# Kernel tuning notes

Hardware: AMD Instinct MI355X
Metric: run time of the kernel (lower is better)

## Reference

```python
import jax, jax.numpy as jnp
import numpy as np

EMBED = 768
HEADS = 12
HEAD_DIM = EMBED // HEADS


def setup_inputs() -> dict:
    key = jax.random.key(0)
    ks = jax.random.split(key, 9)
    B, S, E = 2, 2048, EMBED
    scale = 1.0 / np.sqrt(E)
    return {
        "query": jax.random.normal(ks[0], (B, S, E), jnp.float32),
        "key": jax.random.normal(ks[1], (B, S, E), jnp.float32),
        "value": jax.random.normal(ks[2], (B, S, E), jnp.float32),
        # nn.Linear weights are [out, in]; applied as x @ W.T + b
        "Wq": jax.random.normal(ks[3], (E, E), jnp.float32) * scale,
        "bq": jax.random.normal(ks[4], (E,), jnp.float32) * 0.01,
        "Wk": jax.random.normal(ks[5], (E, E), jnp.float32) * scale,
        "bk": jax.random.normal(ks[6], (E,), jnp.float32) * 0.01,
        "Wv": jax.random.normal(ks[7], (E, E), jnp.float32) * scale,
        "bv": jax.random.normal(ks[8], (E,), jnp.float32) * 0.01,
    }


def reference(query, key, value, Wq, bq, Wk, bk, Wv, bv):
    B, S, E = query.shape
    H, D = HEADS, HEAD_DIM
    # QKV projections (nn.Linear: x @ W.T + b), split into heads
    Q = (query @ Wq.T + bq).reshape(B, S, H, D)
    K = (key @ Wk.T + bk).reshape(B, S, H, D)
    V = (value @ Wv.T + bv).reshape(B, S, H, D)
    # hand-rolled attention: scores -> softmax -> weighted sum
    scores = jnp.einsum("bqhd,bkhd->bhqk", Q, K) / jnp.sqrt(jnp.float32(D))
    attn = jax.nn.softmax(scores, axis=-1)
    out = jnp.einsum("bhqk,bkhd->bqhd", attn, V).reshape(B, S, E)
    return out
```

## Files before the change

kernel.cpp:

```cpp
#include <hip/hip_runtime.h>

#define LOG2E 1.4426950408889634f
#define NEGC (-5.0f * LOG2E)

typedef _Float16 half2v __attribute__((ext_vector_type(2)));
typedef _Float16 half4v __attribute__((ext_vector_type(4)));
typedef _Float16 half8v __attribute__((ext_vector_type(8)));
typedef float float4v __attribute__((ext_vector_type(4)));
typedef float float16v __attribute__((ext_vector_type(16)));
typedef unsigned int uint4v __attribute__((ext_vector_type(4)));

#define NX (2 * 2048 * 768)
#define NW (768 * 768)
#define PO_SPLIT (24 * 2048 * 64)

__device__ __forceinline__ void gload_lds16(const _Float16* g, _Float16* l) {
    __builtin_amdgcn_global_load_lds((const __attribute__((address_space(1))) void*)g,
                                     (__attribute__((address_space(3))) void*)l, 16, 0, 0);
}

__global__ __launch_bounds__(256) void cvt6(
    const float* __restrict__ x0, const float* __restrict__ x1, const float* __restrict__ x2,
    const float* __restrict__ w0, const float* __restrict__ w1, const float* __restrict__ w2,
    _Float16* __restrict__ y0, _Float16* __restrict__ y1, _Float16* __restrict__ y2,
    _Float16* __restrict__ y3, _Float16* __restrict__ y4, _Float16* __restrict__ y5)
{
    const int z = blockIdx.y;
    const float* s; _Float16* d; int n;
    switch (z) {
        case 0: s = x0; d = y0; n = NX; break;
        case 1: s = x1; d = y1; n = NX; break;
        case 2: s = x2; d = y2; n = NX; break;
        case 3: s = w0; d = y3; n = NW; break;
        case 4: s = w1; d = y4; n = NW; break;
        default: s = w2; d = y5; n = NW; break;
    }
    const int i = (blockIdx.x * 256 + threadIdx.x) * 8;
    if (i >= n) return;
    float4v a0 = ((const float4v*)(s + i))[0];
    float4v a1 = ((const float4v*)(s + i))[1];
    half8v h = __builtin_shufflevector(__builtin_convertvector(a0, half4v),
                                       __builtin_convertvector(a1, half4v),
                                       0, 1, 2, 3, 4, 5, 6, 7);
    *(half8v*)(d + i) = h;
}

template<int TM, int TN, int AM, int AN, int MODE>
__global__ __launch_bounds__(256) void gemm16(
    const _Float16* __restrict__ Aq, const _Float16* __restrict__ Ak,
    const _Float16* __restrict__ Bq, const _Float16* __restrict__ Bk,
    const float* __restrict__ biasq, const float* __restrict__ biask,
    _Float16* __restrict__ Oq, _Float16* __restrict__ Ok)
{
    const int z = (MODE == 0) ? blockIdx.z : 0;
    const _Float16* A = z ? Ak : Aq;
    const _Float16* B = z ? Bk : Bq;
    const float* bias = z ? biask : biasq;

    __shared__ _Float16 At[TM * 64];
    __shared__ _Float16 Bt[TN * 64];

    const int t    = threadIdx.x;
    const int wave = t >> 6;
    const int lane = t & 63;
    const int quad = lane >> 4;
    const int l16  = lane & 15;
    const int wm   = (wave & 1) * (AM * 16);
    const int wn   = (wave >> 1) * (AN * 16);
    const int m0   = blockIdx.x * TM;
    const int n0   = blockIdx.y * TN;

    float4v acc[AM][AN];
#pragma unroll
    for (int i = 0; i < AM; i++)
#pragma unroll
        for (int j = 0; j < AN; j++) acc[i][j] = (float4v){0.f, 0.f, 0.f, 0.f};

    const _Float16* Asrc = A + (size_t)m0 * 768;
    const _Float16* Bsrc = B + (size_t)n0 * 768;

    for (int k0 = 0; k0 < 768; k0 += 64) {
#pragma unroll
        for (int j = 0; j < TM / 32; j++) {
            const int s = j * 256 + t;
            const int row = s >> 3;
            const int c = (s & 7) ^ (row & 7);
            gload_lds16(Asrc + (size_t)row * 768 + k0 + c * 8, At + s * 8);
        }
#pragma unroll
        for (int j = 0; j < TN / 32; j++) {
            const int s = j * 256 + t;
            const int row = s >> 3;
            const int c = (s & 7) ^ (row & 7);
            gload_lds16(Bsrc + (size_t)row * 768 + k0 + c * 8, Bt + s * 8);
        }
        __syncthreads();

        half8v af[AM][2], bf[AN][2];
#pragma unroll
        for (int i = 0; i < AM; i++) {
            const int ra = wm + i * 16 + l16;
            const int ca = quad ^ (ra & 7);
            af[i][0] = *(const half8v*)(At + ra * 64 + ca * 8);
            af[i][1] = *(const half8v*)(At + ra * 64 + (ca ^ 4) * 8);
        }
#pragma unroll
        for (int j = 0; j < AN; j++) {
            const int rb = wn + j * 16 + l16;
            const int cb = quad ^ (rb & 7);
            bf[j][0] = *(const half8v*)(Bt + rb * 64 + cb * 8);
            bf[j][1] = *(const half8v*)(Bt + rb * 64 + (cb ^ 4) * 8);
        }
#pragma unroll
        for (int i = 0; i < AM; i++)
#pragma unroll
            for (int j = 0; j < AN; j++) {
                acc[i][j] = __builtin_amdgcn_mfma_f32_16x16x32_f16(af[i][0], bf[j][0], acc[i][j], 0, 0, 0);
                acc[i][j] = __builtin_amdgcn_mfma_f32_16x16x32_f16(af[i][1], bf[j][1], acc[i][j], 0, 0, 0);
            }
        __syncthreads();
    }

    if (MODE == 0) {
        _Float16* O = z ? Ok : Oq;
        const float scale = z ? 1.0f : 0.125f * LOG2E;
#pragma unroll
        for (int j = 0; j < AN; j++) {
            const int col = n0 + wn + j * 16 + l16;
            const float bc = bias[col];
#pragma unroll
            for (int i = 0; i < AM; i++) {
                const int rowb = m0 + wm + i * 16 + quad * 4;
#pragma unroll
                for (int r = 0; r < 4; r++)
                    O[(size_t)(rowb + r) * 768 + col] = (_Float16)((acc[i][j][r] + bc) * scale);
            }
        }
    } else {
#pragma unroll
        for (int i = 0; i < AM; i++) {
#pragma unroll
            for (int r = 0; r < 4; r++) {
                const int m = m0 + wm + i * 16 + quad * 4 + r;
                const float bc = bias[m];
#pragma unroll
                for (int j = 0; j < AN; j++) {
                    const int n = n0 + wn + j * 16 + l16;
                    Oq[((size_t)(n >> 11) * 768 + m) * 2048 + (n & 2047)] = (_Float16)(acc[i][j][r] + bc);
                }
            }
        }
    }
}

__global__ __launch_bounds__(256) void attn3(
    const _Float16* __restrict__ Qh,
    const _Float16* __restrict__ Kh,
    const _Float16* __restrict__ Vt,
    _Float16* __restrict__ Po,
    float* __restrict__ lo)
{
    __shared__ _Float16 smem[4][64 * 64];

    const int t    = threadIdx.x;
    const int wave = t >> 6;
    const int lane = t & 63;
    const int hi   = lane >> 5;
    const int l32  = lane & 31;
    const int q0   = blockIdx.x * 128;
    const int bh   = blockIdx.y;
    const int sp   = blockIdx.z;
    const int b    = bh / 12;
    const int h    = bh % 12;
    const int qw   = q0 + wave * 32;

    const _Float16* qp = Qh + (size_t)(b * 2048 + qw + l32) * 768 + h * 64 + hi * 8;
    half8v qf[4];
#pragma unroll
    for (int d = 0; d < 4; d++) qf[d] = *(const half8v*)(qp + d * 16);

    float16v ot[2];
#pragma unroll
    for (int dc = 0; dc < 2; dc++)
#pragma unroll
        for (int r = 0; r < 16; r++) ot[dc][r] = 0.f;
    float lpart = 0.f;

    const _Float16* Kbase = Kh + (size_t)(b * 2048 + sp * 1024) * 768 + h * 64;
    const _Float16* Vbase = Vt + (size_t)(bh * 64) * 2048 + sp * 1024;

    auto stage = [&](int pp, int kt0) {
#pragma unroll
        for (int j = 0; j < 2; j++) {
            const int s = j * 256 + t;
            const int row = s >> 3;
            const int cg = (s & 7) ^ (row & 7);
            gload_lds16(Kbase + (size_t)(kt0 + row) * 768 + cg * 8, &smem[pp][s * 8]);
            gload_lds16(Vbase + (size_t)row * 2048 + kt0 + cg * 8, &smem[2 + pp][s * 8]);
        }
    };

    stage(0, 0);
    int p = 0;

    for (int it = 0; it < 16; it++) {
        __syncthreads();
        if (it < 15) stage(p ^ 1, (it + 1) * 64);

        float16v st[2];
#pragma unroll
        for (int kc = 0; kc < 2; kc++)
#pragma unroll
            for (int r = 0; r < 16; r++) st[kc][r] = 0.f;
#pragma unroll
        for (int ds = 0; ds < 4; ds++) {
#pragma unroll
            for (int kc = 0; kc < 2; kc++) {
                const int row = kc * 32 + l32;
                const int slot = ((ds << 1) | hi) ^ (row & 7);
                half8v kf = *(const half8v*)(&smem[p][row * 64 + slot * 8]);
                st[kc] = __builtin_amdgcn_mfma_f32_32x32x16_f16(kf, qf[ds], st[kc], 0, 0, 0);
            }
        }

        unsigned int pk[2][8];
#pragma unroll
        for (int kc = 0; kc < 2; kc++)
#pragma unroll
            for (int rp = 0; rp < 8; rp++) {
                const float e0 = __builtin_amdgcn_exp2f(st[kc][2 * rp]     + NEGC);
                const float e1 = __builtin_amdgcn_exp2f(st[kc][2 * rp + 1] + NEGC);
                lpart += e0;
                lpart += e1;
                half2v hp; hp.x = (_Float16)e0; hp.y = (_Float16)e1;
                pk[kc][rp] = __builtin_bit_cast(unsigned int, hp);
            }

#pragma unroll
        for (int ks = 0; ks < 4; ks++) {
            const int kc = ks >> 1;
            const int sb = (ks & 1) * 4;
            const unsigned int d0 = pk[kc][sb], d1 = pk[kc][sb + 1];
            const unsigned int d2 = pk[kc][sb + 2], d3 = pk[kc][sb + 3];
            const unsigned int x = hi ? d0 : d2;
            const unsigned int y = hi ? d1 : d3;
            const unsigned int ex = (unsigned int)__shfl_xor((int)x, 32);
            const unsigned int ey = (unsigned int)__shfl_xor((int)y, 32);
            uint4v bu;
            bu.x = hi ? ex : d0; bu.y = hi ? ey : d1;
            bu.z = hi ? d2 : ex; bu.w = hi ? d3 : ey;
            const half8v pf = __builtin_bit_cast(half8v, bu);
#pragma unroll
            for (int dc = 0; dc < 2; dc++) {
                const int row = dc * 32 + l32;
                const int slot = ((ks << 1) | hi) ^ (row & 7);
                half8v vf = *(const half8v*)(&smem[2 + p][row * 64 + slot * 8]);
                ot[dc] = __builtin_amdgcn_mfma_f32_32x32x16_f16(vf, pf, ot[dc], 0, 0, 0);
            }
        }
        p ^= 1;
    }

    __syncthreads();
    const float l = lpart + __shfl_xor(lpart, 32);
    if (hi == 0)
        lo[(size_t)(sp * 24 + bh) * 2048 + qw + l32] = l;

    float* fo = (float*)(&smem[0][0]) + wave * 2048;
#pragma unroll
    for (int dc = 0; dc < 2; dc++)
#pragma unroll
        for (int g = 0; g < 4; g++) {
            float4v v;
#pragma unroll
            for (int r = 0; r < 4; r++) v[r] = ot[dc][4 * g + r];
            const int c = dc * 8 + 2 * g + hi;
            const int cs = c ^ (l32 & 15);
            *(float4v*)(fo + l32 * 64 + cs * 4) = v;
        }
    const int r4 = lane >> 4, li = lane & 15;
    _Float16* prow = Po + (size_t)(sp * 24 + bh) * 2048 * 64 + (size_t)qw * 64;
#pragma unroll
    for (int pass = 0; pass < 8; pass++) {
        const int qq = pass * 4 + r4;
        float4v v = *(const float4v*)(fo + qq * 64 + (li ^ (qq & 15)) * 4);
        *(half4v*)(prow + (size_t)qq * 64 + li * 4) = __builtin_convertvector(v, half4v);
    }
}

__global__ __launch_bounds__(256) void combine2(
    const _Float16* __restrict__ Po, const float* __restrict__ lo,
    float* __restrict__ out)
{
    const int tid = blockIdx.x * 256 + threadIdx.x;
    const int idx = tid * 4;
    const int d = idx & 63;
    const int r = idx >> 6;
    const int h = r % 12;
    const int t2 = r / 12;
    const int q = t2 & 2047;
    const int b = t2 >> 11;
    const int bh = b * 12 + h;

    const size_t pbase = ((size_t)bh * 2048 + q) * 64 + d;
    float4v p0 = __builtin_convertvector(*(const half4v*)(Po + pbase), float4v);
    float4v p1 = __builtin_convertvector(*(const half4v*)(Po + PO_SPLIT + pbase), float4v);
    const float l0 = lo[(size_t)bh * 2048 + q];
    const float l1 = lo[24 * 2048 + (size_t)bh * 2048 + q];
    const float inv = 1.0f / (l0 + l1);
    float4v v;
#pragma unroll
    for (int i = 0; i < 4; i++) v[i] = (p0[i] + p1[i]) * inv;
    *(float4v*)(out + idx) = v;
}

extern "C" void kernel_launch(void* const* d_in, const int* in_sizes, int n_in,
                              void* d_out, int out_size, void* d_ws, size_t ws_size,
                              hipStream_t stream) {
    const float* q  = (const float*)d_in[0];
    const float* k  = (const float*)d_in[1];
    const float* v  = (const float*)d_in[2];
    const float* Wq = (const float*)d_in[3];
    const float* bq = (const float*)d_in[4];
    const float* Wk = (const float*)d_in[5];
    const float* bk = (const float*)d_in[6];
    const float* Wv = (const float*)d_in[7];
    const float* bv = (const float*)d_in[8];
    float* out = (float*)d_out;

    _Float16* ws   = (_Float16*)d_ws;
    _Float16* Qh   = ws;
    _Float16* Kh   = Qh + NX;
    _Float16* Vth  = Kh + NX;
    _Float16* Xq16 = Vth + NX;
    _Float16* Xk16 = Xq16 + NX;
    _Float16* Xv16 = Xk16 + NX;
    _Float16* Wq16 = Xv16 + NX;
    _Float16* Wk16 = Wq16 + NW;
    _Float16* Wv16 = Wk16 + NW;
    _Float16* Po   = Xq16;
    float*    lo   = (float*)(Po + 2 * PO_SPLIT);

    cvt6<<<dim3(1536, 6), 256, 0, stream>>>(q, k, v, Wq, Wk, Wv,
                                            Xq16, Xk16, Xv16, Wq16, Wk16, Wv16);
    gemm16<64, 96, 2, 3, 0><<<dim3(64, 8, 2), 256, 0, stream>>>(
        Xq16, Xk16, Wq16, Wk16, bq, bk, Qh, Kh);
    gemm16<96, 64, 3, 2, 1><<<dim3(8, 64, 1), 256, 0, stream>>>(
        Wv16, nullptr, Xv16, nullptr, bv, nullptr, Vth, nullptr);
    attn3<<<dim3(16, 24, 2), 256, 0, stream>>>(Qh, Kh, Vth, Po, lo);
    combine2<<<dim3(3072), 256, 0, stream>>>(Po, lo, out);
}
```

Measured before the change: 180.2 us.

## Merge QKV projection GEMMs into one launch and compute softmax row sums via MFMA

Folds the Q/K projection GEMM and the transposed V projection GEMM into a single kernel launch whose grid z dimension selects among the three. This removes one launch and lets all three projections run together on the device. In the attention kernel, the per-lane scalar accumulation of exp values is replaced by an extra MFMA against a vector of ones, which produces the row sums of the fp16-rounded probabilities. This drops the scalar adds and the cross-lane shuffle, but adds one MFMA per k-step and sixteen accumulator registers. It also switches the fp16 conversion to packed round-toward-zero.

```diff
diff --git a/kernel.cpp b/kernel.cpp
--- a/kernel.cpp
+++ b/kernel.cpp
@@ -46,20 +46,11 @@
 }
 
 template<int TM, int TN, int AM, int AN, int MODE>
-__global__ __launch_bounds__(256) void gemm16(
-    const _Float16* __restrict__ Aq, const _Float16* __restrict__ Ak,
-    const _Float16* __restrict__ Bq, const _Float16* __restrict__ Bk,
-    const float* __restrict__ biasq, const float* __restrict__ biask,
-    _Float16* __restrict__ Oq, _Float16* __restrict__ Ok)
-{
-    const int z = (MODE == 0) ? blockIdx.z : 0;
-    const _Float16* A = z ? Ak : Aq;
-    const _Float16* B = z ? Bk : Bq;
-    const float* bias = z ? biask : biasq;
-
-    __shared__ _Float16 At[TM * 64];
-    __shared__ _Float16 Bt[TN * 64];
-
+__device__ __forceinline__ void gemm_body(
+    const _Float16* __restrict__ A, const _Float16* __restrict__ B,
+    const float* __restrict__ bias, _Float16* __restrict__ O,
+    float scale, int m0, int n0, _Float16* At, _Float16* Bt)
+{
     const int t    = threadIdx.x;
     const int wave = t >> 6;
     const int lane = t & 63;
@@ -67,8 +58,6 @@
     const int l16  = lane & 15;
     const int wm   = (wave & 1) * (AM * 16);
     const int wn   = (wave >> 1) * (AN * 16);
-    const int m0   = blockIdx.x * TM;
-    const int n0   = blockIdx.y * TN;
 
     float4v acc[AM][AN];
 #pragma unroll
@@ -122,8 +111,6 @@
     }
 
     if (MODE == 0) {
-        _Float16* O = z ? Ok : Oq;
-        const float scale = z ? 1.0f : 0.125f * LOG2E;
 #pragma unroll
         for (int j = 0; j < AN; j++) {
             const int col = n0 + wn + j * 16 + l16;
@@ -146,11 +133,30 @@
 #pragma unroll
                 for (int j = 0; j < AN; j++) {
                     const int n = n0 + wn + j * 16 + l16;
-                    Oq[((size_t)(n >> 11) * 768 + m) * 2048 + (n & 2047)] = (_Float16)(acc[i][j][r] + bc);
+                    O[((size_t)(n >> 11) * 768 + m) * 2048 + (n & 2047)] = (_Float16)(acc[i][j][r] + bc);
                 }
             }
         }
     }
+}
+
+__global__ __launch_bounds__(256) void gemm_all(
+    const _Float16* __restrict__ Xq, const _Float16* __restrict__ Xk, const _Float16* __restrict__ Xv,
+    const _Float16* __restrict__ Wq, const _Float16* __restrict__ Wk, const _Float16* __restrict__ Wv,
+    const float* __restrict__ bq, const float* __restrict__ bk, const float* __restrict__ bv,
+    _Float16* __restrict__ Oq, _Float16* __restrict__ Ok, _Float16* __restrict__ Ovt)
+{
+    __shared__ _Float16 smem[160 * 64];
+    const int z = blockIdx.z;
+    if (z == 0)
+        gemm_body<64, 96, 2, 3, 0>(Xq, Wq, bq, Oq, 0.125f * LOG2E,
+                                   blockIdx.x * 64, blockIdx.y * 96, smem, smem + 64 * 64);
+    else if (z == 1)
+        gemm_body<64, 96, 2, 3, 0>(Xk, Wk, bk, Ok, 1.0f,
+                                   blockIdx.x * 64, blockIdx.y * 96, smem, smem + 64 * 64);
+    else
+        gemm_body<96, 64, 3, 2, 1>(Wv, Xv, bv, Ovt, 1.0f,
+                                   blockIdx.y * 96, blockIdx.x * 64, smem, smem + 96 * 64);
 }
 
 __global__ __launch_bounds__(256) void attn3(
@@ -179,12 +185,17 @@
 #pragma unroll
     for (int d = 0; d < 4; d++) qf[d] = *(const half8v*)(qp + d * 16);
 
-    float16v ot[2];
+    half8v onesA;
+#pragma unroll
+    for (int j = 0; j < 8; j++) onesA[j] = (_Float16)1.0f;
+
+    float16v ot[2], otl;
 #pragma unroll
     for (int dc = 0; dc < 2; dc++)
 #pragma unroll
         for (int r = 0; r < 16; r++) ot[dc][r] = 0.f;
-    float lpart = 0.f;
+#pragma unroll
+    for (int r = 0; r < 16; r++) otl[r] = 0.f;
 
     const _Float16* Kbase = Kh + (size_t)(b * 2048 + sp * 1024) * 768 + h * 64;
     const _Float16* Vbase = Vt + (size_t)(bh * 64) * 2048 + sp * 1024;
@@ -230,9 +241,7 @@
             for (int rp = 0; rp < 8; rp++) {
                 const float e0 = __builtin_amdgcn_exp2f(st[kc][2 * rp]     + NEGC);
                 const float e1 = __builtin_amdgcn_exp2f(st[kc][2 * rp + 1] + NEGC);
-                lpart += e0;
-                lpart += e1;
-                half2v hp; hp.x = (_Float16)e0; hp.y = (_Float16)e1;
+                auto hp = __builtin_amdgcn_cvt_pkrtz(e0, e1);
                 pk[kc][rp] = __builtin_bit_cast(unsigned int, hp);
             }
 
@@ -257,14 +266,14 @@
                 half8v vf = *(const half8v*)(&smem[2 + p][row * 64 + slot * 8]);
                 ot[dc] = __builtin_amdgcn_mfma_f32_32x32x16_f16(vf, pf, ot[dc], 0, 0, 0);
             }
+            otl = __builtin_amdgcn_mfma_f32_32x32x16_f16(onesA, pf, otl, 0, 0, 0);
         }
         p ^= 1;
     }
 
     __syncthreads();
-    const float l = lpart + __shfl_xor(lpart, 32);
     if (hi == 0)
-        lo[(size_t)(sp * 24 + bh) * 2048 + qw + l32] = l;
+        lo[(size_t)(sp * 24 + bh) * 2048 + qw + l32] = otl[0];
 
     float* fo = (float*)(&smem[0][0]) + wave * 2048;
 #pragma unroll
@@ -343,10 +352,8 @@
 
     cvt6<<<dim3(1536, 6), 256, 0, stream>>>(q, k, v, Wq, Wk, Wv,
                                             Xq16, Xk16, Xv16, Wq16, Wk16, Wv16);
-    gemm16<64, 96, 2, 3, 0><<<dim3(64, 8, 2), 256, 0, stream>>>(
-        Xq16, Xk16, Wq16, Wk16, bq, bk, Qh, Kh);
-    gemm16<96, 64, 3, 2, 1><<<dim3(8, 64, 1), 256, 0, stream>>>(
-        Wv16, nullptr, Xv16, nullptr, bv, nullptr, Vth, nullptr);
+    gemm_all<<<dim3(64, 8, 3), 256, 0, stream>>>(
+        Xq16, Xk16, Xv16, Wq16, Wk16, Wv16, bq, bk, bv, Qh, Kh, Vth);
     attn3<<<dim3(16, 24, 2), 256, 0, stream>>>(Qh, Kh, Vth, Po, lo);
     combine2<<<dim3(3072), 256, 0, stream>>>(Po, lo, out);
 }
```

Result: faster. 170.2 us (-5.5%).
